# Optimization experiments

Hardware: AMD Instinct MI355X
Metric: run time of the kernel (lower is better)

## Reference

```python
import jax, jax.numpy as jnp
import numpy as np

SS, D, V = 64, 256, 10000
B, S = 16, 512


def setup_inputs() -> dict:
    key = jax.random.key(0)
    ks = jax.random.split(key, 7)
    scale = lambda fan_in: 1.0 / np.sqrt(fan_in)
    return {
        "x": jax.random.normal(ks[0], (B, S, D), dtype=jnp.float32),
        # nn.Linear(D, 4*ss): weight [4ss, D], bias [4ss]
        "Wxs_w": jax.random.uniform(ks[1], (4 * SS, D), jnp.float32, -scale(D), scale(D)),
        "Wxs_b": jax.random.uniform(ks[2], (4 * SS,), jnp.float32, -scale(D), scale(D)),
        # nn.Linear(ss, 4*ss)
        "Wss_w": jax.random.uniform(ks[3], (4 * SS, SS), jnp.float32, -scale(SS), scale(SS)),
        "Wss_b": jax.random.uniform(ks[4], (4 * SS,), jnp.float32, -scale(SS), scale(SS)),
        # nn.Linear(ss, V)
        "Wsy_w": jax.random.uniform(ks[5], (V, SS), jnp.float32, -scale(SS), scale(SS)),
        "Wsy_b": jax.random.uniform(ks[6], (V,), jnp.float32, -scale(SS), scale(SS)),
    }


def reference(x, Wxs_w, Wxs_b, Wss_w, Wss_b, Wsy_w, Wsy_b):
    b, s, _ = x.shape
    ss = Wss_w.shape[1]
    # Precompute input projections for all timesteps: [s, b, 4ss]
    xproj = jnp.einsum("bsd,kd->sbk", x, Wxs_w) + Wxs_b

    def step(carry, xp_t):
        h, c = carry
        comb = xp_t + h @ Wss_w.T + Wss_b  # [b, 4ss]
        f, i, g, o = jnp.split(comb, 4, axis=-1)
        f = jax.nn.sigmoid(f)
        i = jax.nn.sigmoid(i)
        o = jax.nn.sigmoid(o)
        g = jnp.tanh(g)
        c = c * f + i * g
        h = o * c  # NOTE: original code omits tanh(c) here; stay faithful
        return (h, c), h

    h0 = jnp.zeros((b, ss), dtype=x.dtype)
    c0 = jnp.zeros((b, ss), dtype=x.dtype)
    _, hs = jax.lax.scan(step, (h0, c0), xproj)  # hs: [s, b, ss]
    # Per-step vocab projection == batched projection of stacked hidden states
    y = jnp.einsum("sbh,vh->bsv", hs, Wsy_w) + Wsy_b  # [b, s, V]
    return y
```

## Files before the change

kernel.cpp:

```cpp
#include <hip/hip_runtime.h>

typedef unsigned short u16;
typedef unsigned int u32;

using short8 = __attribute__((ext_vector_type(8))) short;
using f32x4  = __attribute__((ext_vector_type(4))) float;
using f32x2  = __attribute__((ext_vector_type(2))) float;

#define SSEQ 512
#define BB   16
#define DD   256
#define G4   256
#define SSZ  64
#define VV   10000
#define VPAD 10112
#define MALL 8192

#define OFF_XHI   0u
#define OFF_XLO   4194304u
#define OFF_WHI   8388608u
#define OFF_WLO   8519680u
#define OFF_WSY   8650752u
#define OFF_XPROJ 9945088u
#define OFF_HS    18333696u

__device__ __forceinline__ u16 f2bf(float f) {
  u32 u = __float_as_uint(f);
  u32 r = (u + 0x7fffu + ((u >> 16) & 1u)) >> 16;
  return (u16)r;
}
__device__ __forceinline__ float bf2f(u16 h) {
  return __uint_as_float(((u32)h) << 16);
}
__device__ __forceinline__ f32x2 pkfma(f32x2 a, f32x2 b, f32x2 c) {
  asm("v_pk_fma_f32 %0, %1, %2, %0" : "+v"(c) : "v"(a), "v"(b));
  return c;
}
template <int CTRL>
__device__ __forceinline__ float qadd(float x) {
  int pv = __builtin_amdgcn_update_dpp(0, __float_as_int(x), CTRL, 0xf, 0xf, true);
  return x + __int_as_float(pv);
}

#define NX 2097152
#define NW 65536
#define NP 647168
__global__ void k0_convert(const float* __restrict__ x, const float* __restrict__ Wxs,
                           const float* __restrict__ Wsy,
                           u16* __restrict__ xhi, u16* __restrict__ xlo,
                           u16* __restrict__ whi, u16* __restrict__ wlo,
                           u16* __restrict__ wsyb) {
  int i = blockIdx.x * 256 + threadIdx.x;
  if (i < NX) {
    float v = x[i]; u16 h = f2bf(v);
    xhi[i] = h; xlo[i] = f2bf(v - bf2f(h));
  } else if (i < NX + NW) {
    int j = i - NX;
    float v = Wxs[j]; u16 h = f2bf(v);
    whi[j] = h; wlo[j] = f2bf(v - bf2f(h));
  } else if (i < NX + NW + NP) {
    int j = i - NX - NW;
    wsyb[j] = (j < VV * SSZ) ? f2bf(Wsy[j]) : (u16)0;
  }
}

__global__ __launch_bounds__(256) void k1_xproj(
    const u16* __restrict__ xhi, const u16* __restrict__ xlo,
    const u16* __restrict__ whi, const u16* __restrict__ wlo,
    const float* __restrict__ bias, float* __restrict__ xproj) {
  int bid = blockIdx.x;
  int mb = bid >> 1, nb = bid & 1;
  int tid = threadIdx.x, l = tid & 63, wid = tid >> 6;
  int wm = wid >> 1, wv = wid & 1;
  int m0 = mb * 128 + wm * 64, n0 = nb * 128 + wv * 64;
  int lr = l & 15, lg = l >> 4;

  f32x4 acc[4][4];
#pragma unroll
  for (int a = 0; a < 4; a++)
#pragma unroll
    for (int bq = 0; bq < 4; bq++) acc[a][bq] = (f32x4){0.f, 0.f, 0.f, 0.f};

#pragma unroll
  for (int p = 0; p < 3; p++) {
    const u16* A = (p == 1) ? xlo : xhi;
    const u16* B = (p == 2) ? wlo : whi;
#pragma unroll
    for (int ks = 0; ks < 8; ks++) {
      short8 af[4], bf_[4];
#pragma unroll
      for (int fm = 0; fm < 4; fm++)
        af[fm] = *(const short8*)(A + (size_t)(m0 + fm * 16 + lr) * 256 + ks * 32 + lg * 8);
#pragma unroll
      for (int fv = 0; fv < 4; fv++)
        bf_[fv] = *(const short8*)(B + (size_t)(n0 + fv * 16 + lr) * 256 + ks * 32 + lg * 8);
#pragma unroll
      for (int fm = 0; fm < 4; fm++)
#pragma unroll
        for (int fv = 0; fv < 4; fv++)
          acc[fm][fv] = __builtin_amdgcn_mfma_f32_16x16x32_bf16(af[fm], bf_[fv], acc[fm][fv], 0, 0, 0);
    }
  }
#pragma unroll
  for (int fv = 0; fv < 4; fv++) {
    int j = n0 + fv * 16 + lr;
    float bj = bias[j];
#pragma unroll
    for (int fm = 0; fm < 4; fm++)
#pragma unroll
      for (int r = 0; r < 4; r++) {
        int m = m0 + fm * 16 + lg * 4 + r;
        xproj[(size_t)m * 256 + j] = acc[fm][fv][r] + bj;
      }
  }
}

__global__ __launch_bounds__(256, 1) void k2_scan(
    const float* __restrict__ xproj, const float* __restrict__ Wss,
    const float* __restrict__ Wssb, u16* __restrict__ hsb) {
  __shared__ float hbuf[2][64];
  __shared__ u16 hstage[SSEQ][64];

  int b = blockIdx.x, tid = threadIdx.x;
  int w = tid >> 6, l = tid & 63;
  int oo = l >> 2, ks = l & 3;
  int jj = w * 16 + oo;

  f32x2 wr[32];
  float bias4[4];
#pragma unroll
  for (int g = 0; g < 4; g++) {
    const f32x2* pw = (const f32x2*)(Wss + (size_t)(g * 64 + jj) * 64 + ks * 16);
#pragma unroll
    for (int q = 0; q < 8; q++) wr[g * 8 + q] = pw[q];
    bias4[g] = Wssb[g * 64 + jj];
  }

  const float* xpb = xproj + (size_t)b * SSEQ * 256 + jj;
  float xpc[4], xpn[4];
#pragma unroll
  for (int g = 0; g < 4; g++) xpc[g] = xpb[g * 64];

  if (tid < 128) ((float*)hbuf)[tid] = 0.f;
  __syncthreads();

  float c = 0.f;

  for (int t = 0; t < SSEQ; t++) {
    int rb = (t + 1) & 1;
    f32x4 h4[4];
    const f32x4* hb = (const f32x4*)&hbuf[rb][ks * 16];
    h4[0] = hb[0]; h4[1] = hb[1]; h4[2] = hb[2]; h4[3] = hb[3];

    if (t + 1 < SSEQ) {
      const float* xn = xpb + (size_t)(t + 1) * 256;
#pragma unroll
      for (int g = 0; g < 4; g++) xpn[g] = xn[g * 64];
    }

    float p[4];
#pragma unroll
    for (int g = 0; g < 4; g++) {
      f32x2 a0 = (f32x2){0.f, 0.f}, a1 = (f32x2){0.f, 0.f};
#pragma unroll
      for (int q = 0; q < 4; q++) {
        f32x2 hA = (f32x2){h4[q][0], h4[q][1]};
        f32x2 hB = (f32x2){h4[q][2], h4[q][3]};
        a0 = pkfma(hA, wr[g * 8 + 2 * q], a0);
        a1 = pkfma(hB, wr[g * 8 + 2 * q + 1], a1);
      }
      p[g] = (a0[0] + a0[1]) + (a1[0] + a1[1]);
    }

#pragma unroll
    for (int g = 0; g < 4; g++) p[g] = qadd<0x4E>(qadd<0xB1>(p[g]));

    float pf = p[0] + xpc[0] + bias4[0];
    float pi = p[1] + xpc[1] + bias4[1];
    float pg = p[2] + xpc[2] + bias4[2];
    float po = p[3] + xpc[3] + bias4[3];

    float fg = __builtin_amdgcn_rcpf(1.f + exp2f(-1.442695041f * pf));
    float ig = __builtin_amdgcn_rcpf(1.f + exp2f(-1.442695041f * pi));
    float og = __builtin_amdgcn_rcpf(1.f + exp2f(-1.442695041f * po));
    float gg = fmaf(-2.f, __builtin_amdgcn_rcpf(exp2f(2.885390082f * pg) + 1.f), 1.f);

    c = fmaf(c, fg, ig * gg);
    float hn = og * c;

    if (ks == 0) {
      hbuf[t & 1][jj] = hn;
      hstage[t][jj] = f2bf(hn);
    }
    asm volatile("s_waitcnt lgkmcnt(0)\n\ts_barrier" ::: "memory");

#pragma unroll
    for (int g = 0; g < 4; g++) xpc[g] = xpn[g];
  }

  __syncthreads();
  const uint4* src = (const uint4*)hstage;
  uint4* dst = (uint4*)(hsb + (size_t)b * SSEQ * 64);
#pragma unroll
  for (int i = 0; i < 16; i++) dst[tid + 256 * i] = src[tid + 256 * i];
}

__global__ __launch_bounds__(256) void k3_y(
    const u16* __restrict__ hsb, const u16* __restrict__ wsyb,
    const float* __restrict__ bias, float* __restrict__ y) {
  int bid = blockIdx.x;
  int mb = bid / 79, vb = bid - mb * 79;
  int tid = threadIdx.x, l = tid & 63, wid = tid >> 6;
  int wm = wid >> 1, wv = wid & 1;
  int m0 = mb * 128 + wm * 64, v0 = vb * 128 + wv * 64;
  int lr = l & 15, lg = l >> 4;

  f32x4 acc[4][4];
#pragma unroll
  for (int a = 0; a < 4; a++)
#pragma unroll
    for (int bq = 0; bq < 4; bq++) acc[a][bq] = (f32x4){0.f, 0.f, 0.f, 0.f};

#pragma unroll
  for (int ks = 0; ks < 2; ks++) {
    short8 af[4], bf_[4];
#pragma unroll
    for (int fm = 0; fm < 4; fm++)
      af[fm] = *(const short8*)(hsb + (size_t)(m0 + fm * 16 + lr) * 64 + ks * 32 + lg * 8);
#pragma unroll
    for (int fv = 0; fv < 4; fv++)
      bf_[fv] = *(const short8*)(wsyb + (size_t)(v0 + fv * 16 + lr) * 64 + ks * 32 + lg * 8);
#pragma unroll
    for (int fv = 0; fv < 4; fv++)
#pragma unroll
      for (int fm = 0; fm < 4; fm++)
        acc[fv][fm] = __builtin_amdgcn_mfma_f32_16x16x32_bf16(bf_[fv], af[fm], acc[fv][fm], 0, 0, 0);
  }

#pragma unroll
  for (int fv = 0; fv < 4; fv++) {
    int vb4 = v0 + fv * 16 + lg * 4;
    bool ok = (vb4 + 3) < VV;
    float4 bv = ok ? *(const float4*)(bias + vb4) : float4{0.f, 0.f, 0.f, 0.f};
#pragma unroll
    for (int fm = 0; fm < 4; fm++) {
      int m = m0 + fm * 16 + lr;
      if (ok) {
        float4 o;
        o.x = acc[fv][fm][0] + bv.x;
        o.y = acc[fv][fm][1] + bv.y;
        o.z = acc[fv][fm][2] + bv.z;
        o.w = acc[fv][fm][3] + bv.w;
        *(float4*)(y + (size_t)m * (size_t)VV + vb4) = o;
      }
    }
  }
}

extern "C" void kernel_launch(void* const* d_in, const int* in_sizes, int n_in,
                              void* d_out, int out_size, void* d_ws, size_t ws_size,
                              hipStream_t stream) {
  const float* x     = (const float*)d_in[0];
  const float* Wxs_w = (const float*)d_in[1];
  const float* Wxs_b = (const float*)d_in[2];
  const float* Wss_w = (const float*)d_in[3];
  const float* Wss_b = (const float*)d_in[4];
  const float* Wsy_w = (const float*)d_in[5];
  const float* Wsy_b = (const float*)d_in[6];
  float* y = (float*)d_out;
  char* ws = (char*)d_ws;

  u16*   xhi   = (u16*)(ws + OFF_XHI);
  u16*   xlo   = (u16*)(ws + OFF_XLO);
  u16*   whi   = (u16*)(ws + OFF_WHI);
  u16*   wlo   = (u16*)(ws + OFF_WLO);
  u16*   wsyb  = (u16*)(ws + OFF_WSY);
  float* xproj = (float*)(ws + OFF_XPROJ);
  u16*   hsb   = (u16*)(ws + OFF_HS);

  k0_convert<<<(NX + NW + NP) / 256, 256, 0, stream>>>(x, Wxs_w, Wsy_w, xhi, xlo, whi, wlo, wsyb);
  k1_xproj<<<128, 256, 0, stream>>>(xhi, xlo, whi, wlo, Wxs_b, xproj);
  k2_scan<<<16, 256, 0, stream>>>(xproj, Wss_w, Wss_b, hsb);
  k3_y<<<64 * 79, 256, 0, stream>>>(hsb, wsyb, Wsy_b, y);
}
```

Before: 315.5 us.

## Run LSTM scan as one block using split-bf16 MFMA over all batches

The recurrent scan now runs in a single workgroup that handles all 16 batch rows together. The h·Wss^T recurrence is computed with 16x16x32 bf16 MFMA instructions, using a hi/lo bf16 split of both h and Wss (three products) to keep close to fp32 accuracy. Wss is pre-split in the convert kernel, and hidden states are written straight to global memory each step instead of being staged in shared memory. This replaces per-row VALU dot products and DPP reductions with matrix instructions, at the cost of running on only one CU and adding MFMA latency to the serial critical path of each timestep.

```diff
diff --git a/kernel.cpp b/kernel.cpp
--- a/kernel.cpp
+++ b/kernel.cpp
@@ -5,7 +5,6 @@
 
 using short8 = __attribute__((ext_vector_type(8))) short;
 using f32x4  = __attribute__((ext_vector_type(4))) float;
-using f32x2  = __attribute__((ext_vector_type(2))) float;
 
 #define SSEQ 512
 #define BB   16
@@ -23,6 +22,8 @@
 #define OFF_WSY   8650752u
 #define OFF_XPROJ 9945088u
 #define OFF_HS    18333696u
+#define OFF_WSSH  19382272u
+#define OFF_WSSL  19415040u
 
 __device__ __forceinline__ u16 f2bf(float f) {
   u32 u = __float_as_uint(f);
@@ -32,24 +33,17 @@
 __device__ __forceinline__ float bf2f(u16 h) {
   return __uint_as_float(((u32)h) << 16);
 }
-__device__ __forceinline__ f32x2 pkfma(f32x2 a, f32x2 b, f32x2 c) {
-  asm("v_pk_fma_f32 %0, %1, %2, %0" : "+v"(c) : "v"(a), "v"(b));
-  return c;
-}
-template <int CTRL>
-__device__ __forceinline__ float qadd(float x) {
-  int pv = __builtin_amdgcn_update_dpp(0, __float_as_int(x), CTRL, 0xf, 0xf, true);
-  return x + __int_as_float(pv);
-}
 
 #define NX 2097152
 #define NW 65536
 #define NP 647168
+#define NS 16384
 __global__ void k0_convert(const float* __restrict__ x, const float* __restrict__ Wxs,
-                           const float* __restrict__ Wsy,
+                           const float* __restrict__ Wsy, const float* __restrict__ Wss,
                            u16* __restrict__ xhi, u16* __restrict__ xlo,
                            u16* __restrict__ whi, u16* __restrict__ wlo,
-                           u16* __restrict__ wsyb) {
+                           u16* __restrict__ wsyb,
+                           u16* __restrict__ wssh, u16* __restrict__ wssl) {
   int i = blockIdx.x * 256 + threadIdx.x;
   if (i < NX) {
     float v = x[i]; u16 h = f2bf(v);
@@ -61,6 +55,10 @@
   } else if (i < NX + NW + NP) {
     int j = i - NX - NW;
     wsyb[j] = (j < VV * SSZ) ? f2bf(Wsy[j]) : (u16)0;
+  } else if (i < NX + NW + NP + NS) {
+    int j = i - NX - NW - NP;
+    float v = Wss[j]; u16 h = f2bf(v);
+    wssh[j] = h; wssl[j] = f2bf(v - bf2f(h));
   }
 }
 
@@ -116,93 +114,100 @@
 }
 
 __global__ __launch_bounds__(256, 1) void k2_scan(
-    const float* __restrict__ xproj, const float* __restrict__ Wss,
+    const float* __restrict__ xproj,
+    const u16* __restrict__ wssh, const u16* __restrict__ wssl,
     const float* __restrict__ Wssb, u16* __restrict__ hsb) {
-  __shared__ float hbuf[2][64];
-  __shared__ u16 hstage[SSEQ][64];
-
-  int b = blockIdx.x, tid = threadIdx.x;
+  __shared__ u16 hbh[2][16][72];
+  __shared__ u16 hbl[2][16][72];
+
+  int tid = threadIdx.x;
   int w = tid >> 6, l = tid & 63;
-  int oo = l >> 2, ks = l & 3;
-  int jj = w * 16 + oo;
-
-  f32x2 wr[32];
-  float bias4[4];
-#pragma unroll
-  for (int g = 0; g < 4; g++) {
-    const f32x2* pw = (const f32x2*)(Wss + (size_t)(g * 64 + jj) * 64 + ks * 16);
-#pragma unroll
-    for (int q = 0; q < 8; q++) wr[g * 8 + q] = pw[q];
-    bias4[g] = Wssb[g * 64 + jj];
-  }
-
-  const float* xpb = xproj + (size_t)b * SSEQ * 256 + jj;
-  float xpc[4], xpn[4];
-#pragma unroll
-  for (int g = 0; g < 4; g++) xpc[g] = xpb[g * 64];
-
-  if (tid < 128) ((float*)hbuf)[tid] = 0.f;
+  int lr = l & 15, lg = l >> 4;
+
+  short8 wh[4][2], wl[4][2];
+#pragma unroll
+  for (int g = 0; g < 4; g++)
+#pragma unroll
+    for (int s = 0; s < 2; s++) {
+      int n = g * 64 + w * 16 + lr;
+      wh[g][s] = *(const short8*)(wssh + n * 64 + s * 32 + lg * 8);
+      wl[g][s] = *(const short8*)(wssl + n * 64 + s * 32 + lg * 8);
+    }
+  float bcol[4];
+#pragma unroll
+  for (int g = 0; g < 4; g++) bcol[g] = Wssb[g * 64 + w * 16 + lr];
+
+  const float* xbase = xproj + w * 16 + lr;
+  float xpc[4][4], xpn[4][4];
+#pragma unroll
+  for (int g = 0; g < 4; g++)
+#pragma unroll
+    for (int r = 0; r < 4; r++)
+      xpc[g][r] = xbase[((size_t)(lg * 4 + r) * SSEQ + 0) * 256 + g * 64];
+
+  for (int i = tid; i < 16 * 72; i += 256) {
+    hbh[0][0][i] = 0; hbh[1][0][i] = 0;
+    hbl[0][0][i] = 0; hbl[1][0][i] = 0;
+  }
   __syncthreads();
 
-  float c = 0.f;
+  float c[4] = {0.f, 0.f, 0.f, 0.f};
+  u16* hout = hsb + w * 16 + lr;
 
   for (int t = 0; t < SSEQ; t++) {
-    int rb = (t + 1) & 1;
-    f32x4 h4[4];
-    const f32x4* hb = (const f32x4*)&hbuf[rb][ks * 16];
-    h4[0] = hb[0]; h4[1] = hb[1]; h4[2] = hb[2]; h4[3] = hb[3];
+    int rb = (t + 1) & 1, wb = t & 1;
+
+    short8 ah[2], al[2];
+#pragma unroll
+    for (int s = 0; s < 2; s++) {
+      ah[s] = *(const short8*)(&hbh[rb][lr][s * 32 + lg * 8]);
+      al[s] = *(const short8*)(&hbl[rb][lr][s * 32 + lg * 8]);
+    }
 
     if (t + 1 < SSEQ) {
-      const float* xn = xpb + (size_t)(t + 1) * 256;
-#pragma unroll
-      for (int g = 0; g < 4; g++) xpn[g] = xn[g * 64];
-    }
-
-    float p[4];
-#pragma unroll
-    for (int g = 0; g < 4; g++) {
-      f32x2 a0 = (f32x2){0.f, 0.f}, a1 = (f32x2){0.f, 0.f};
-#pragma unroll
-      for (int q = 0; q < 4; q++) {
-        f32x2 hA = (f32x2){h4[q][0], h4[q][1]};
-        f32x2 hB = (f32x2){h4[q][2], h4[q][3]};
-        a0 = pkfma(hA, wr[g * 8 + 2 * q], a0);
-        a1 = pkfma(hB, wr[g * 8 + 2 * q + 1], a1);
+#pragma unroll
+      for (int g = 0; g < 4; g++)
+#pragma unroll
+        for (int r = 0; r < 4; r++)
+          xpn[g][r] = xbase[((size_t)(lg * 4 + r) * SSEQ + (t + 1)) * 256 + g * 64];
+    }
+
+    f32x4 acc[4];
+#pragma unroll
+    for (int g = 0; g < 4; g++)
+      acc[g] = (f32x4){xpc[g][0] + bcol[g], xpc[g][1] + bcol[g],
+                       xpc[g][2] + bcol[g], xpc[g][3] + bcol[g]};
+
+#pragma unroll
+    for (int g = 0; g < 4; g++)
+#pragma unroll
+      for (int s = 0; s < 2; s++) {
+        acc[g] = __builtin_amdgcn_mfma_f32_16x16x32_bf16(ah[s], wh[g][s], acc[g], 0, 0, 0);
+        acc[g] = __builtin_amdgcn_mfma_f32_16x16x32_bf16(al[s], wh[g][s], acc[g], 0, 0, 0);
+        acc[g] = __builtin_amdgcn_mfma_f32_16x16x32_bf16(ah[s], wl[g][s], acc[g], 0, 0, 0);
       }
-      p[g] = (a0[0] + a0[1]) + (a1[0] + a1[1]);
-    }
-
-#pragma unroll
-    for (int g = 0; g < 4; g++) p[g] = qadd<0x4E>(qadd<0xB1>(p[g]));
-
-    float pf = p[0] + xpc[0] + bias4[0];
-    float pi = p[1] + xpc[1] + bias4[1];
-    float pg = p[2] + xpc[2] + bias4[2];
-    float po = p[3] + xpc[3] + bias4[3];
-
-    float fg = __builtin_amdgcn_rcpf(1.f + exp2f(-1.442695041f * pf));
-    float ig = __builtin_amdgcn_rcpf(1.f + exp2f(-1.442695041f * pi));
-    float og = __builtin_amdgcn_rcpf(1.f + exp2f(-1.442695041f * po));
-    float gg = fmaf(-2.f, __builtin_amdgcn_rcpf(exp2f(2.885390082f * pg) + 1.f), 1.f);
-
-    c = fmaf(c, fg, ig * gg);
-    float hn = og * c;
-
-    if (ks == 0) {
-      hbuf[t & 1][jj] = hn;
-      hstage[t][jj] = f2bf(hn);
+
+#pragma unroll
+    for (int r = 0; r < 4; r++) {
+      float fg = __builtin_amdgcn_rcpf(1.f + exp2f(-1.442695041f * acc[0][r]));
+      float ig = __builtin_amdgcn_rcpf(1.f + exp2f(-1.442695041f * acc[1][r]));
+      float gg = fmaf(-2.f, __builtin_amdgcn_rcpf(exp2f(2.885390082f * acc[2][r]) + 1.f), 1.f);
+      float og = __builtin_amdgcn_rcpf(1.f + exp2f(-1.442695041f * acc[3][r]));
+      c[r] = fmaf(c[r], fg, ig * gg);
+      float hn = og * c[r];
+      u16 hh = f2bf(hn);
+      u16 hl = f2bf(hn - bf2f(hh));
+      hbh[wb][lg * 4 + r][w * 16 + lr] = hh;
+      hbl[wb][lg * 4 + r][w * 16 + lr] = hl;
+      hout[((size_t)(lg * 4 + r) * SSEQ + t) * 64] = hh;
     }
     asm volatile("s_waitcnt lgkmcnt(0)\n\ts_barrier" ::: "memory");
 
 #pragma unroll
-    for (int g = 0; g < 4; g++) xpc[g] = xpn[g];
-  }
-
-  __syncthreads();
-  const uint4* src = (const uint4*)hstage;
-  uint4* dst = (uint4*)(hsb + (size_t)b * SSEQ * 64);
-#pragma unroll
-  for (int i = 0; i < 16; i++) dst[tid + 256 * i] = src[tid + 256 * i];
+    for (int g = 0; g < 4; g++)
+#pragma unroll
+      for (int r = 0; r < 4; r++) xpc[g][r] = xpn[g][r];
+  }
 }
 
 __global__ __launch_bounds__(256) void k3_y(
@@ -277,9 +282,12 @@
   u16*   wsyb  = (u16*)(ws + OFF_WSY);
   float* xproj = (float*)(ws + OFF_XPROJ);
   u16*   hsb   = (u16*)(ws + OFF_HS);
-
-  k0_convert<<<(NX + NW + NP) / 256, 256, 0, stream>>>(x, Wxs_w, Wsy_w, xhi, xlo, whi, wlo, wsyb);
+  u16*   wssh  = (u16*)(ws + OFF_WSSH);
+  u16*   wssl  = (u16*)(ws + OFF_WSSL);
+
+  k0_convert<<<(NX + NW + NP + NS) / 256, 256, 0, stream>>>(
+      x, Wxs_w, Wsy_w, Wss_w, xhi, xlo, whi, wlo, wsyb, wssh, wssl);
   k1_xproj<<<128, 256, 0, stream>>>(xhi, xlo, whi, wlo, Wxs_b, xproj);
-  k2_scan<<<16, 256, 0, stream>>>(xproj, Wss_w, Wss_b, hsb);
+  k2_scan<<<1, 256, 0, stream>>>(xproj, wssh, wssl, Wss_b, hsb);
   k3_y<<<64 * 79, 256, 0, stream>>>(hsb, wsyb, Wsy_b, y);
 }
```

Measured after the change: 615.8 us. +95.2%, slower.
